# Kernel tuning notes

Measured on AMD Instinct MI355X. Metric: run time of the kernel, lower is better.

Reference implementation:

```python
import jax, jax.numpy as jnp
import numpy as np

K = 3          # kernel size (implied by 18/27 offset channels)
PAD = 1
STRIDE = 1


def setup_inputs() -> dict:
    key = jax.random.key(0)
    k0, k1, k2 = jax.random.split(key, 3)
    B, C, H, W = 4, 256, 64, 64
    Cout = 256
    x = jax.random.normal(k0, (B, C, H, W), jnp.float32)
    # offset/mask predicting conv: 18 offset + 9 mask channels (deform_group=1)
    w_off = jax.random.normal(k1, (27, C, K, K), jnp.float32) * 0.01
    b_off = jnp.zeros((27,), jnp.float32)
    # main deformable conv weight (bias=False)
    w = jax.random.normal(k2, (Cout, C, K, K), jnp.float32) * 0.05
    return {"x": x, "w_off": w_off, "b_off": b_off, "w": w}


def _modulated_dcn(x, w_off, b_off, w):
    B, C, H, W = x.shape
    KK = K * K
    # regular conv predicting offsets (+ mask)
    om = jax.lax.conv_general_dilated(
        x, w_off, (STRIDE, STRIDE), [(PAD, PAD), (PAD, PAD)],
        dimension_numbers=("NCHW", "OIHW", "NCHW")) + b_off[None, :, None, None]
    Ho, Wo = om.shape[2], om.shape[3]
    # channel layout: interleaved (dy, dx) per kernel tap, then 9 mask channels
    off = om[:, :2 * KK].reshape(B, KK, 2, Ho, Wo)
    mask = jax.nn.sigmoid(om[:, 2 * KK:3 * KK])            # (B, KK, Ho, Wo)

    ky, kx = jnp.meshgrid(jnp.arange(K), jnp.arange(K), indexing="ij")
    base_y = (jnp.arange(Ho) * STRIDE - PAD)[:, None]       # (Ho, 1)
    base_x = (jnp.arange(Wo) * STRIDE - PAD)[None, :]       # (1, Wo)
    # sampling positions p = p0 + pn + offset, shape (B, KK, Ho, Wo)
    py = base_y[None, None] + ky.reshape(KK)[None, :, None, None] + off[:, :, 0]
    px = base_x[None, None] + kx.reshape(KK)[None, :, None, None] + off[:, :, 1]

    y0f = jnp.floor(py)
    x0f = jnp.floor(px)
    ly = py - y0f
    lx = px - x0f
    y0 = y0f.astype(jnp.int32)
    x0 = x0f.astype(jnp.int32)

    xf = x.reshape(B, C, H * W)

    def samp(yi, xi):
        valid = ((yi >= 0) & (yi < H) & (xi >= 0) & (xi < W)).astype(x.dtype)
        idx = jnp.clip(yi, 0, H - 1) * W + jnp.clip(xi, 0, W - 1)
        v = jnp.take_along_axis(xf, idx.reshape(B, 1, -1), axis=2)
        return v.reshape(B, C, KK, Ho, Wo) * valid[:, None]

    # bilinear interpolation with zero padding outside the image
    v = (samp(y0,     x0    ) * ((1 - ly) * (1 - lx))[:, None]
         + samp(y0,     x0 + 1) * ((1 - ly) * lx)[:, None]
         + samp(y0 + 1, x0    ) * (ly * (1 - lx))[:, None]
         + samp(y0 + 1, x0 + 1) * (ly * lx)[:, None])
    v = v * mask[:, None]                                   # modulation
    # conv as contraction over (Cin, KK)
    return jnp.einsum("bckhw,ock->bohw", v, w.reshape(w.shape[0], C, KK))


def reference(x, w_off, b_off, w):
    return _modulated_dcn(x, w_off, b_off, w)
```

## Files before the change

kernel.cpp:

```cpp
#include <hip/hip_runtime.h>
#include <math.h>

#define HH 64
#define WW 64
#define CIN 256
#define COUT 256
#define KKT 9
#define HWSZ 4096
#define VP 260

typedef __bf16  v8bf   __attribute__((ext_vector_type(8)));
typedef float   v4f    __attribute__((ext_vector_type(4)));
typedef short   short8 __attribute__((ext_vector_type(8)));
typedef unsigned short ushort4v __attribute__((ext_vector_type(4)));

__device__ inline unsigned short f2bf(float f) {
    union { float f; unsigned u; } uf; uf.f = f;
    unsigned r = uf.u + 0x7fff + ((uf.u >> 16) & 1);
    return (unsigned short)(r >> 16);
}
__device__ inline float bf2f(unsigned short u) {
    union { unsigned u; float f; } uf; uf.u = ((unsigned)u) << 16;
    return uf.f;
}

__global__ __launch_bounds__(256) void k_prep(const float* __restrict__ x,
                                              const float* __restrict__ w,
                                              const float* __restrict__ w_off,
                                              unsigned short* __restrict__ x_t,
                                              unsigned short* __restrict__ wprep,
                                              unsigned short* __restrict__ woffp) {
    __shared__ float s_w[2304];
    int id  = blockIdx.x;
    int tid = threadIdx.x;
    if (id < 256) {
        int b  = id >> 6;
        int h  = id & 63;
        int px  = tid & 63;
        int oct = tid >> 6;
        const float* xr = x + (((size_t)b * CIN) * HH + h) * WW;
        unsigned short* orow = x_t + (((size_t)id) * WW + px) * CIN;
        for (int g = 0; g < 8; g++) {
            int cb = g * 32 + oct * 8;
            unsigned short v[8];
#pragma unroll
            for (int j = 0; j < 8; j++)
                v[j] = f2bf(xr[(size_t)(cb + j) * HWSZ + px]);
            *(short8*)(orow + cb) = *(short8*)v;
        }
    } else if (id < 512) {
        int o = id - 256;
        for (int i = tid; i < 2304; i += 256) s_w[i] = w[(size_t)o * 2304 + i];
        __syncthreads();
        for (int u = tid; u < 576; u += 256) {
            int t  = u >> 3;
            int kq = u & 7;
            unsigned short v[4];
#pragma unroll
            for (int j = 0; j < 4; j++) {
                int kp = t * 32 + kq * 4 + j;
                int kk = kp >> 8;
                int c  = kp & 255;
                v[j] = f2bf(s_w[c * 9 + kk]);
            }
            *(ushort4v*)&wprep[((size_t)(t * 256 + o)) * 32 + kq * 4] = *(ushort4v*)v;
        }
    } else {
        int t = id - 512;
#pragma unroll
        for (int i = 0; i < 4; i++) {
            int idx = i * 256 + tid;
            int och = idx >> 5;
            int ki  = idx & 31;
            int kp  = t * 32 + ki;
            int kk  = kp >> 8;
            int c   = kp & 255;
            float v = (och < 27) ? w_off[((size_t)och * 256 + c) * 9 + kk] : 0.f;
            woffp[(size_t)t * 1024 + idx] = f2bf(v);
        }
    }
}

__global__ __launch_bounds__(512, 4) void k_main(const unsigned short* __restrict__ x_t,
                                                 const unsigned short* __restrict__ wprep,
                                                 const unsigned short* __restrict__ woffp,
                                                 const float* __restrict__ b_off,
                                                 float* __restrict__ out) {
    int id    = blockIdx.x;
    int g     = id & 7;
    int phalf = (id >> 3) & 1;
    int hi    = (id >> 4) & 7;
    int b     = id >> 7;
    int h     = g * 8 + hi;
    int p0    = phalf * 32;
    int tid  = threadIdx.x;
    int lane = tid & 63;
    int oct  = tid >> 6;
    int m16  = lane & 15;
    int quad = lane >> 4;

    __shared__ __align__(16) unsigned short s_reg[3 * 34 * VP];
    __shared__ int4   s_base[KKT][32];
    __shared__ float4 s_wt  [KKT][32];
    __shared__ float  s_om  [27][33];

    const unsigned short* xb = x_t + (size_t)b * HWSZ * CIN;

    for (int u = tid; u < 3 * 1088; u += 512) {
        int row = u / 1088;
        int rem = u - row * 1088;
        int px  = rem >> 5;
        int c8  = (rem & 31) * 8;
        int y   = h + row - 1;
        int xg  = p0 + px - 1;
        short8 val = (short8)0;
        if ((unsigned)y < HH && (unsigned)xg < WW)
            val = *(const short8*)(xb + ((size_t)y * WW + xg) * CIN + c8);
        *(short8*)&s_reg[(row * 34 + px) * VP + c8] = val;
    }
    __syncthreads();

    {
        int g2  = oct >> 1;
        int ntw = oct & 1;
        v4f oa[2];
        oa[0] = (v4f)(0.f);
        oa[1] = (v4f)(0.f);
#pragma unroll
        for (int ky = 0; ky < 3; ky++)
#pragma unroll
        for (int kx = 0; kx < 3; kx++)
#pragma unroll
        for (int c2 = 0; c2 < 2; c2++) {
            int ch = c2 * 4 + g2;
            int t  = (ky * 3 + kx) * 8 + ch;
            const unsigned short* wp = woffp + (size_t)t * 1024;
            short8 af0 = *(const short8*)(wp + m16 * 32 + quad * 8);
            short8 af1 = *(const short8*)(wp + (16 + m16) * 32 + quad * 8);
            short8 bfr = *(const short8*)
                &s_reg[(ky * 34 + ntw * 16 + m16 + kx) * VP + ch * 32 + quad * 8];
            oa[0] = __builtin_amdgcn_mfma_f32_16x16x32_bf16(
                __builtin_bit_cast(v8bf, af0), __builtin_bit_cast(v8bf, bfr), oa[0], 0, 0, 0);
            oa[1] = __builtin_amdgcn_mfma_f32_16x16x32_bf16(
                __builtin_bit_cast(v8bf, af1), __builtin_bit_cast(v8bf, bfr), oa[1], 0, 0, 0);
        }
        __syncthreads();
        float* s_red = (float*)s_reg;
#pragma unroll
        for (int mt = 0; mt < 2; mt++)
#pragma unroll
            for (int r = 0; r < 4; r++)
                s_red[(g2 * 32 + mt * 16 + quad * 4 + r) * 33 + ntw * 16 + m16] = oa[mt][r];
        __syncthreads();
        for (int i2 = tid; i2 < 27 * 32; i2 += 512) {
            int och = i2 >> 5;
            int px  = i2 & 31;
            float s = s_red[och * 33 + px]         + s_red[(32 + och) * 33 + px]
                    + s_red[(64 + och) * 33 + px]  + s_red[(96 + och) * 33 + px]
                    + b_off[och];
            s_om[och][px] = s;
        }
        __syncthreads();
    }

    for (int i = tid; i < KKT * 32; i += 512) {
        int kk = i >> 5;
        int pl = i & 31;
        int p  = p0 + pl;
        float offy = s_om[2 * kk][pl];
        float offx = s_om[2 * kk + 1][pl];
        float mv   = s_om[18 + kk][pl];
        int ky = kk / 3, kx = kk - 3 * (kk / 3);
        float py = (float)(h - 1 + ky) + offy;
        float px = (float)(p - 1 + kx) + offx;
        float y0f = floorf(py);
        float x0f = floorf(px);
        float ly = py - y0f, lx = px - x0f;
        int y0 = (int)y0f, x0 = (int)x0f;
        float m = 1.f / (1.f + __expf(-mv));
        bool yv0 = (unsigned)y0       < HH;
        bool yv1 = (unsigned)(y0 + 1) < HH;
        bool xv0 = (unsigned)x0       < WW;
        bool xv1 = (unsigned)(x0 + 1) < WW;
        int y0c = min(max(y0, 0), HH - 1);
        int y1c = min(max(y0 + 1, 0), HH - 1);
        int x0c = min(max(x0, 0), WW - 1);
        int x1c = min(max(x0 + 1, 0), WW - 1);
        s_base[kk][pl] = make_int4((y0c * WW + x0c) * CIN, (y0c * WW + x1c) * CIN,
                                   (y1c * WW + x0c) * CIN, (y1c * WW + x1c) * CIN);
        s_wt[kk][pl] = make_float4(
            (yv0 && xv0) ? (1.f - ly) * (1.f - lx) * m : 0.f,
            (yv0 && xv1) ? (1.f - ly) * lx         * m : 0.f,
            (yv1 && xv0) ? ly * (1.f - lx)         * m : 0.f,
            (yv1 && xv1) ? ly * lx                 * m : 0.f);
    }
    __syncthreads();

    v4f acc[2][2];
#pragma unroll
    for (int mt = 0; mt < 2; mt++)
#pragma unroll
        for (int nt = 0; nt < 2; nt++) acc[mt][nt] = (v4f)(0.f);

    const unsigned short* xc = xb + lane * 4;

    ushort4v tt[4][4];
#pragma unroll
    for (int i = 0; i < 4; i++) {
        int4 bp = s_base[0][oct * 4 + i];
        tt[i][0] = *(const ushort4v*)(xc + bp.x);
        tt[i][1] = *(const ushort4v*)(xc + bp.y);
        tt[i][2] = *(const ushort4v*)(xc + bp.z);
        tt[i][3] = *(const ushort4v*)(xc + bp.w);
    }

#pragma unroll
    for (int kk = 0; kk < KKT; kk++) {
        unsigned short* sv = s_reg + (kk & 1) * (32 * VP);

#pragma unroll
        for (int i = 0; i < 4; i++) {
            int pl = oct * 4 + i;
            float4 wt = s_wt[kk][pl];
            unsigned short vv[4];
#pragma unroll
            for (int j = 0; j < 4; j++) {
                float val = wt.x * bf2f(tt[i][0][j]) + wt.y * bf2f(tt[i][1][j])
                          + wt.z * bf2f(tt[i][2][j]) + wt.w * bf2f(tt[i][3][j]);
                vv[j] = f2bf(val);
            }
            *(ushort4v*)&sv[pl * VP + lane * 4] = *(ushort4v*)vv;
        }

        if (kk < KKT - 1) {
#pragma unroll
            for (int i = 0; i < 4; i++) {
                int4 bp = s_base[kk + 1][oct * 4 + i];
                tt[i][0] = *(const ushort4v*)(xc + bp.x);
                tt[i][1] = *(const ushort4v*)(xc + bp.y);
                tt[i][2] = *(const ushort4v*)(xc + bp.z);
                tt[i][3] = *(const ushort4v*)(xc + bp.w);
            }
        }

        asm volatile("s_waitcnt lgkmcnt(0)" ::: "memory");
        __builtin_amdgcn_s_barrier();
        __builtin_amdgcn_sched_barrier(0);

#pragma unroll 2
        for (int ch = 0; ch < 8; ch++) {
            int t = kk * 8 + ch;
            const unsigned short* wp = wprep + ((size_t)t * 256 + oct * 32) * 32;
            short8 af0 = *(const short8*)(wp + m16 * 32 + quad * 8);
            short8 af1 = *(const short8*)(wp + (16 + m16) * 32 + quad * 8);
            short8 bfr[2];
#pragma unroll
            for (int nt = 0; nt < 2; nt++)
                bfr[nt] = *(const short8*)&sv[(nt * 16 + m16) * VP + ch * 32 + quad * 8];
#pragma unroll
            for (int nt = 0; nt < 2; nt++) {
                acc[0][nt] = __builtin_amdgcn_mfma_f32_16x16x32_bf16(
                    __builtin_bit_cast(v8bf, af0), __builtin_bit_cast(v8bf, bfr[nt]),
                    acc[0][nt], 0, 0, 0);
                acc[1][nt] = __builtin_amdgcn_mfma_f32_16x16x32_bf16(
                    __builtin_bit_cast(v8bf, af1), __builtin_bit_cast(v8bf, bfr[nt]),
                    acc[1][nt], 0, 0, 0);
            }
        }
    }

    float* ob = out + ((size_t)b * COUT) * HWSZ + h * WW + p0;
#pragma unroll
    for (int mt = 0; mt < 2; mt++)
#pragma unroll
        for (int nt = 0; nt < 2; nt++)
#pragma unroll
            for (int r = 0; r < 4; r++) {
                int o = oct * 32 + mt * 16 + quad * 4 + r;
                ob[(size_t)o * HWSZ + nt * 16 + m16] = acc[mt][nt][r];
            }
}

extern "C" void kernel_launch(void* const* d_in, const int* in_sizes, int n_in,
                              void* d_out, int out_size, void* d_ws, size_t ws_size,
                              hipStream_t stream) {
    const float* x     = (const float*)d_in[0];
    const float* w_off = (const float*)d_in[1];
    const float* b_off = (const float*)d_in[2];
    const float* w     = (const float*)d_in[3];
    float* out = (float*)d_out;

    unsigned short* x_t   = (unsigned short*)d_ws;
    unsigned short* wprep = x_t + (size_t)4 * HWSZ * CIN;
    unsigned short* woffp = wprep + 589824;

    hipLaunchKernelGGL(k_prep, dim3(584), dim3(256), 0, stream, x, w, w_off, x_t, wprep, woffp);
    hipLaunchKernelGGL(k_main, dim3(512), dim3(512), 0, stream, x_t, wprep, woffp, b_off, out);
}
```

Measured before the change: 168.8 us.

## Transpose x through LDS in prep and drop double-buffered sampling pipeline

The prep kernel now transposes x into channel-last bf16 via a padded shared-memory tile, using float4 coalesced reads and 16-byte writes in place of strided per-channel loads. It launches twice as many blocks, each covering half a row. The main kernel drops the register prefetch of the next tap's bilinear corners and the LDS double buffer. It now uses a single buffer with two __syncthreads per tap, which cuts register and LDS pressure but serializes gather latency with the MFMA loop.

```diff
diff --git a/kernel.cpp b/kernel.cpp
--- a/kernel.cpp
+++ b/kernel.cpp
@@ -8,6 +8,7 @@
 #define KKT 9
 #define HWSZ 4096
 #define VP 260
+#define TP 264
 
 typedef __bf16  v8bf   __attribute__((ext_vector_type(8)));
 typedef float   v4f    __attribute__((ext_vector_type(4)));
@@ -30,26 +31,38 @@
                                               unsigned short* __restrict__ x_t,
                                               unsigned short* __restrict__ wprep,
                                               unsigned short* __restrict__ woffp) {
-    __shared__ float s_w[2304];
+    __shared__ __align__(16) unsigned short s_t[32 * TP];
     int id  = blockIdx.x;
     int tid = threadIdx.x;
-    if (id < 256) {
-        int b  = id >> 6;
-        int h  = id & 63;
-        int px  = tid & 63;
-        int oct = tid >> 6;
-        const float* xr = x + (((size_t)b * CIN) * HH + h) * WW;
-        unsigned short* orow = x_t + (((size_t)id) * WW + px) * CIN;
-        for (int g = 0; g < 8; g++) {
-            int cb = g * 32 + oct * 8;
-            unsigned short v[8];
-#pragma unroll
-            for (int j = 0; j < 8; j++)
-                v[j] = f2bf(xr[(size_t)(cb + j) * HWSZ + px]);
-            *(short8*)(orow + cb) = *(short8*)v;
-        }
-    } else if (id < 512) {
-        int o = id - 256;
+    if (id < 512) {
+        int b    = id >> 7;
+        int r    = id & 127;
+        int h    = r >> 1;
+        int half = r & 1;
+        const float* xr = x + ((size_t)b * CIN) * HWSZ + h * WW + half * 32;
+#pragma unroll
+        for (int it = 0; it < 8; it++) {
+            int idx = it * 256 + tid;
+            int c   = idx >> 3;
+            int p4  = idx & 7;
+            float4 v = *(const float4*)(xr + (size_t)c * HWSZ + p4 * 4);
+            s_t[(p4 * 4 + 0) * TP + c] = f2bf(v.x);
+            s_t[(p4 * 4 + 1) * TP + c] = f2bf(v.y);
+            s_t[(p4 * 4 + 2) * TP + c] = f2bf(v.z);
+            s_t[(p4 * 4 + 3) * TP + c] = f2bf(v.w);
+        }
+        __syncthreads();
+        unsigned short* orow = x_t + (((size_t)(b * 64 + h)) * WW + half * 32) * CIN;
+#pragma unroll
+        for (int it = 0; it < 4; it++) {
+            int idx = it * 256 + tid;
+            int px  = idx >> 5;
+            int c8  = (idx & 31) * 8;
+            *(short8*)(orow + (size_t)px * CIN + c8) = *(const short8*)&s_t[px * TP + c8];
+        }
+    } else if (id < 768) {
+        float* s_w = (float*)s_t;
+        int o = id - 512;
         for (int i = tid; i < 2304; i += 256) s_w[i] = w[(size_t)o * 2304 + i];
         __syncthreads();
         for (int u = tid; u < 576; u += 256) {
@@ -66,7 +79,7 @@
             *(ushort4v*)&wprep[((size_t)(t * 256 + o)) * 32 + kq * 4] = *(ushort4v*)v;
         }
     } else {
-        int t = id - 512;
+        int t = id - 768;
 #pragma unroll
         for (int i = 0; i < 4; i++) {
             int idx = i * 256 + tid;
@@ -203,49 +216,28 @@
         for (int nt = 0; nt < 2; nt++) acc[mt][nt] = (v4f)(0.f);
 
     const unsigned short* xc = xb + lane * 4;
-
-    ushort4v tt[4][4];
-#pragma unroll
-    for (int i = 0; i < 4; i++) {
-        int4 bp = s_base[0][oct * 4 + i];
-        tt[i][0] = *(const ushort4v*)(xc + bp.x);
-        tt[i][1] = *(const ushort4v*)(xc + bp.y);
-        tt[i][2] = *(const ushort4v*)(xc + bp.z);
-        tt[i][3] = *(const ushort4v*)(xc + bp.w);
-    }
-
-#pragma unroll
+    unsigned short* s_v = s_reg;
+
     for (int kk = 0; kk < KKT; kk++) {
-        unsigned short* sv = s_reg + (kk & 1) * (32 * VP);
-
 #pragma unroll
         for (int i = 0; i < 4; i++) {
             int pl = oct * 4 + i;
+            int4   bp = s_base[kk][pl];
             float4 wt = s_wt[kk][pl];
+            ushort4v t0 = *(const ushort4v*)(xc + bp.x);
+            ushort4v t1 = *(const ushort4v*)(xc + bp.y);
+            ushort4v t2 = *(const ushort4v*)(xc + bp.z);
+            ushort4v t3 = *(const ushort4v*)(xc + bp.w);
             unsigned short vv[4];
 #pragma unroll
             for (int j = 0; j < 4; j++) {
-                float val = wt.x * bf2f(tt[i][0][j]) + wt.y * bf2f(tt[i][1][j])
-                          + wt.z * bf2f(tt[i][2][j]) + wt.w * bf2f(tt[i][3][j]);
+                float val = wt.x * bf2f(t0[j]) + wt.y * bf2f(t1[j])
+                          + wt.z * bf2f(t2[j]) + wt.w * bf2f(t3[j]);
                 vv[j] = f2bf(val);
             }
-            *(ushort4v*)&sv[pl * VP + lane * 4] = *(ushort4v*)vv;
-        }
-
-        if (kk < KKT - 1) {
-#pragma unroll
-            for (int i = 0; i < 4; i++) {
-                int4 bp = s_base[kk + 1][oct * 4 + i];
-                tt[i][0] = *(const ushort4v*)(xc + bp.x);
-                tt[i][1] = *(const ushort4v*)(xc + bp.y);
-                tt[i][2] = *(const ushort4v*)(xc + bp.z);
-                tt[i][3] = *(const ushort4v*)(xc + bp.w);
-            }
-        }
-
-        asm volatile("s_waitcnt lgkmcnt(0)" ::: "memory");
-        __builtin_amdgcn_s_barrier();
-        __builtin_amdgcn_sched_barrier(0);
+            *(ushort4v*)&s_v[pl * VP + lane * 4] = *(ushort4v*)vv;
+        }
+        __syncthreads();
 
 #pragma unroll 2
         for (int ch = 0; ch < 8; ch++) {
@@ -256,7 +248,7 @@
             short8 bfr[2];
 #pragma unroll
             for (int nt = 0; nt < 2; nt++)
-                bfr[nt] = *(const short8*)&sv[(nt * 16 + m16) * VP + ch * 32 + quad * 8];
+                bfr[nt] = *(const short8*)&s_v[(nt * 16 + m16) * VP + ch * 32 + quad * 8];
 #pragma unroll
             for (int nt = 0; nt < 2; nt++) {
                 acc[0][nt] = __builtin_amdgcn_mfma_f32_16x16x32_bf16(
@@ -267,6 +259,7 @@
                     acc[1][nt], 0, 0, 0);
             }
         }
+        __syncthreads();
     }
 
     float* ob = out + ((size_t)b * COUT) * HWSZ + h * WW + p0;
@@ -294,6 +287,6 @@
     unsigned short* wprep = x_t + (size_t)4 * HWSZ * CIN;
     unsigned short* woffp = wprep + 589824;
 
-    hipLaunchKernelGGL(k_prep, dim3(584), dim3(256), 0, stream, x, w, w_off, x_t, wprep, woffp);
+    hipLaunchKernelGGL(k_prep, dim3(840), dim3(256), 0, stream, x, w, w_off, x_t, wprep, woffp);
     hipLaunchKernelGGL(k_main, dim3(512), dim3(512), 0, stream, x_t, wprep, woffp, b_off, out);
 }
```

New measurement: 169.5 us. About the same (+0.4%).
